# Performance work log

Measured on AMD Instinct MI355X. Metric: run time of the kernel, lower is better.

## Reference

```python
import jax, jax.numpy as jnp
import numpy as np

IN_F = 4096
OUT_F = 4096
SPLIT_F = 410   # ceil(4096 * 0.1)
NUM_PARTS = 10  # ceil(4096 / 410)


def setup_inputs() -> dict:
    key = jax.random.key(0)
    ks = jax.random.split(key, 7)
    s = 1.0 / np.sqrt(IN_F)
    sn = 1.0 / np.sqrt(NUM_PARTS)
    return {
        'x': jax.random.normal(ks[0], (2, 2048, IN_F), dtype=jnp.float32),
        'Wsel': jax.random.uniform(ks[1], (NUM_PARTS, IN_F), jnp.float32, -s, s),
        'bsel': jax.random.uniform(ks[2], (NUM_PARTS,), jnp.float32, -s, s),
        'Wexp': jax.random.uniform(ks[3], (IN_F, NUM_PARTS), jnp.float32, -sn, sn),
        'bexp': jax.random.uniform(ks[4], (IN_F,), jnp.float32, -sn, sn),
        'Wfc': jax.random.uniform(ks[5], (SPLIT_F, IN_F), jnp.float32, -s, s),
        'bfc': jax.random.uniform(ks[6], (SPLIT_F,), jnp.float32, -s, s),
        'out_features': OUT_F,
    }


def reference(x, Wsel, bsel, Wexp, bexp, Wfc, bfc, out_features):
    # selector: sx[..., n]
    sx = jnp.einsum('bsi,ni->bsn', x, Wsel) + bsel
    # expander(diag_embed(sx)): px[..., n, f] = sx[..., n] * Wexp[f, n] + bexp[f]
    # (diag matrix never materialized; mathematically identical)
    px = sx[..., :, None] * Wexp.T[None, None, :, :] + bexp  # [b, s, n, in]
    xx = x[..., None, :] + px                                # broadcast-add of x
    y = jnp.einsum('bsni,fi->bsnf', xx, Wfc) + bfc           # splitfc, [b, s, n, sf]
    y = y.reshape(y.shape[0], y.shape[1], -1)                # (n sf) flatten
    return y[..., :out_features]
```

## Files before the change

### kernel.cpp

```cpp
#include <hip/hip_runtime.h>
#include <hip/hip_bf16.h>
#include <stdint.h>

#define TKS    4096
#define KD     4096
#define NSF    410
#define NPARTS 10
#define NPAD   512
#define OUTF   4096

#define BM 64
#define BN 64
#define BK 128

typedef unsigned short u16;
typedef __attribute__((ext_vector_type(8))) short bf16x8;
typedef __attribute__((ext_vector_type(4))) float f32x4;

#define WS_XB  0
#define WS_BSW ((size_t)TKS * KD * 2)
#define WS_G   (WS_BSW + (size_t)NPAD * KD * 2)
#define WS_C   (WS_G + (size_t)NPAD * NPARTS * 4)
#define WS_SX  (WS_C + (size_t)NPAD * 4)
#define WS_WT  (WS_SX + (size_t)TKS * NPARTS * 4)

__device__ inline u16 f2bf(float f) {
    union { __hip_bfloat16 b; u16 u; } cv;
    cv.b = __float2bfloat16(f);
    return cv.u;
}

typedef __attribute__((address_space(3))) unsigned int as3_uint;
typedef __attribute__((address_space(1))) unsigned int as1_uint;
__device__ inline void gl_lds16(const void* g, void* l) {
    __builtin_amdgcn_global_load_lds((as1_uint*)(uintptr_t)g,
                                     (as3_uint*)(uintptr_t)l, 16, 0, 0);
}

__device__ inline int g_row(int g) { int s = g >> 6; return (s >> 2) * 32 + (s & 1) * 16 + (g & 15); }
__device__ inline int g_col(int g) { int s = g >> 6; return ((s >> 1) & 1) * 32 + ((g >> 4) & 3) * 8; }

__global__ __launch_bounds__(256) void retile_x(const float* __restrict__ x,
                                                u16* __restrict__ xb) {
    const int kt = blockIdx.x & 63, tb = blockIdx.x >> 6;
    const int tid = threadIdx.x;
    const float* tin = x + (size_t)(tb * 64) * KD + kt * 64;
    u16* tout = xb + ((size_t)(tb * 64 + kt) * 512) * 8;
#pragma unroll
    for (int j = 0; j < 2; ++j) {
        const int g = j * 256 + tid;
        const int r = g_row(g), cg = g_col(g);
        float4 v0 = *(const float4*)&tin[(size_t)r * KD + cg];
        float4 v1 = *(const float4*)&tin[(size_t)r * KD + cg + 4];
        u16 h[8] = { f2bf(v0.x), f2bf(v0.y), f2bf(v0.z), f2bf(v0.w),
                     f2bf(v1.x), f2bf(v1.y), f2bf(v1.z), f2bf(v1.w) };
        *(uint4*)&tout[(size_t)g * 8] = *(uint4*)h;
    }
}

__global__ __launch_bounds__(256) void retile_b(const float* __restrict__ Wfc,
                                                u16* __restrict__ bsw) {
    const int kt = blockIdx.x & 63, rb = blockIdx.x >> 6;
    const int tid = threadIdx.x;
    u16* tout = bsw + ((size_t)(rb * 64 + kt) * 512) * 8;
#pragma unroll
    for (int j = 0; j < 2; ++j) {
        const int g = j * 256 + tid;
        const int r = rb * 64 + g_row(g);
        uint4 pk = make_uint4(0u, 0u, 0u, 0u);
        if (r < NSF) {
            const float* src = Wfc + (size_t)r * KD + kt * 64 + g_col(g);
            float4 v0 = *(const float4*)src;
            float4 v1 = *(const float4*)(src + 4);
            u16 h[8] = { f2bf(v0.x), f2bf(v0.y), f2bf(v0.z), f2bf(v0.w),
                         f2bf(v1.x), f2bf(v1.y), f2bf(v1.z), f2bf(v1.w) };
            pk = *(uint4*)h;
        }
        *(uint4*)&tout[(size_t)g * 8] = pk;
    }
}

__global__ __launch_bounds__(256) void sel_kernel(const float* __restrict__ x,
                                                  const float* __restrict__ Wsel,
                                                  const float* __restrict__ bsel,
                                                  float* __restrict__ sx) {
    __shared__ float wsl[NPARTS][512];
    const int tid  = threadIdx.x;
    const int lane = tid & 63;
    const int w    = tid >> 6;
    const int t0   = blockIdx.x * 8 + w * 2;

    float acc0[NPARTS], acc1[NPARTS];
#pragma unroll
    for (int n = 0; n < NPARTS; ++n) { acc0[n] = 0.f; acc1[n] = 0.f; }

    const float* xr0 = x + (size_t)t0 * KD;
    const float* xr1 = xr0 + KD;

    for (int ch = 0; ch < 8; ++ch) {
        __syncthreads();
#pragma unroll
        for (int it = 0; it < 5; ++it) {
            int idx = it * 256 + tid;
            int n = idx >> 7, c4 = (idx & 127) * 4;
            *(float4*)&wsl[n][c4] = *(const float4*)&Wsel[n * KD + ch * 512 + c4];
        }
        __syncthreads();
#pragma unroll
        for (int j = 0; j < 2; ++j) {
            int kl = j * 256 + lane * 4;
            float4 x0 = *(const float4*)&xr0[ch * 512 + kl];
            float4 x1 = *(const float4*)&xr1[ch * 512 + kl];
#pragma unroll
            for (int n = 0; n < NPARTS; ++n) {
                float4 wv = *(float4*)&wsl[n][kl];
                acc0[n] += x0.x * wv.x + x0.y * wv.y + x0.z * wv.z + x0.w * wv.w;
                acc1[n] += x1.x * wv.x + x1.y * wv.y + x1.z * wv.z + x1.w * wv.w;
            }
        }
    }
#pragma unroll
    for (int off = 32; off >= 1; off >>= 1)
#pragma unroll
        for (int n = 0; n < NPARTS; ++n) {
            acc0[n] += __shfl_xor(acc0[n], off);
            acc1[n] += __shfl_xor(acc1[n], off);
        }
    if (lane == 0) {
#pragma unroll
        for (int n = 0; n < NPARTS; ++n) {
            float bs = bsel[n];
            sx[(size_t)t0 * NPARTS + n]       = acc0[n] + bs;
            sx[(size_t)(t0 + 1) * NPARTS + n] = acc1[n] + bs;
        }
    }
}

__global__ __launch_bounds__(256) void prep_a(const float* __restrict__ Wexp,
                                              const float* __restrict__ bexp,
                                              float* __restrict__ WT) {
    const int k = blockIdx.x * 256 + threadIdx.x;
#pragma unroll
    for (int n = 0; n < NPARTS; ++n) WT[(size_t)n * KD + k] = Wexp[(size_t)k * NPARTS + n];
    WT[(size_t)NPARTS * KD + k] = bexp[k];
}

__global__ __launch_bounds__(256) void prep_b(const float* __restrict__ Wfc,
                                              const float* __restrict__ bfc,
                                              const float* __restrict__ WT,
                                              float* __restrict__ G,
                                              float* __restrict__ c) {
    const int f = blockIdx.x;
    const int tid = threadIdx.x;
    float acc[NPARTS + 1];
#pragma unroll
    for (int n = 0; n <= NPARTS; ++n) acc[n] = 0.f;

#pragma unroll
    for (int i = 0; i < 4; ++i) {
        const int k = i * 1024 + tid * 4;
        float4 wv = *(const float4*)&Wfc[(size_t)f * KD + k];
#pragma unroll
        for (int n = 0; n <= NPARTS; ++n) {
            float4 t = *(const float4*)&WT[(size_t)n * KD + k];
            acc[n] += wv.x * t.x + wv.y * t.y + wv.z * t.z + wv.w * t.w;
        }
    }
#pragma unroll
    for (int off = 32; off >= 1; off >>= 1)
#pragma unroll
        for (int n = 0; n <= NPARTS; ++n) acc[n] += __shfl_xor(acc[n], off);

    __shared__ float red[4][NPARTS + 1];
    const int w = tid >> 6, lane = tid & 63;
    if (lane == 0) {
#pragma unroll
        for (int n = 0; n <= NPARTS; ++n) red[w][n] = acc[n];
    }
    __syncthreads();
    if (tid < NPARTS)
        G[(size_t)f * NPARTS + tid] = red[0][tid] + red[1][tid] + red[2][tid] + red[3][tid];
    if (tid == NPARTS)
        c[f] = red[0][NPARTS] + red[1][NPARTS] + red[2][NPARTS] + red[3][NPARTS] + bfc[f];
}

__global__ __launch_bounds__(256, 2) void main_kernel(const u16* __restrict__ xb,
                                                      const u16* __restrict__ bsw,
                                                      const float* __restrict__ G,
                                                      const float* __restrict__ cvec,
                                                      const float* __restrict__ sx,
                                                      float* __restrict__ out) {
    __shared__ __align__(16) u16 As[2][8192];
    __shared__ __align__(16) u16 Bs[2][8192];
    __shared__ float sxs[BM][NPARTS];
    __shared__ float Gs[BN][NPARTS];
    __shared__ float cs[BN];

    const int tid = threadIdx.x;
    const int fb  = blockIdx.x >> 6;
    const int tb  = blockIdx.x & 63;

    const int lane = tid & 63;
    const int w  = tid >> 6;
    const int wr = w >> 1, wc = w & 1;
    const int q  = lane >> 4, ml = lane & 15;

    f32x4 acc[2][2];
#pragma unroll
    for (int mi = 0; mi < 2; ++mi)
#pragma unroll
        for (int ni = 0; ni < 2; ++ni) acc[mi][ni] = (f32x4){0.f, 0.f, 0.f, 0.f};

    const u16* abase = xb  + (size_t)tb * 64 * 4096;
    const u16* bbase = bsw + (size_t)fb * 64 * 4096;

    for (int idx = tid; idx < BM * NPARTS; idx += 256)
        sxs[idx / NPARTS][idx % NPARTS] = sx[(size_t)(tb * BM + idx / NPARTS) * NPARTS + idx % NPARTS];
    for (int idx = tid; idx < BN * NPARTS; idx += 256)
        Gs[idx / NPARTS][idx % NPARTS] = G[(size_t)(fb * BN + idx / NPARTS) * NPARTS + idx % NPARTS];
    if (tid < BN) cs[tid] = cvec[fb * BN + tid];

#pragma unroll
    for (int k = 0; k < 4; ++k) {
        gl_lds16(abase + (k * 256 + tid) * 8, &As[0][(k * 256 + tid) * 8]);
        gl_lds16(bbase + (k * 256 + tid) * 8, &Bs[0][(k * 256 + tid) * 8]);
    }
    __syncthreads();

    int buf = 0;
#pragma unroll 2
    for (int it = 0; it < KD / BK; ++it) {
        if (it + 1 < KD / BK) {
            const size_t off = (size_t)(it + 1) * 8192;
#pragma unroll
            for (int k = 0; k < 4; ++k) {
                gl_lds16(abase + off + (k * 256 + tid) * 8, &As[buf ^ 1][(k * 256 + tid) * 8]);
                gl_lds16(bbase + off + (k * 256 + tid) * 8, &Bs[buf ^ 1][(k * 256 + tid) * 8]);
            }
        }
#pragma unroll
        for (int ks = 0; ks < 4; ++ks) {
            const int tb2 = (ks >> 1) * 512;
            const int kl  = ks & 1;
            bf16x8 av[2], bv[2];
#pragma unroll
            for (int mi = 0; mi < 2; ++mi)
                av[mi] = *(const bf16x8*)&As[buf][(tb2 + ((wr * 2 + kl) * 2 + mi) * 64 + lane) * 8];
#pragma unroll
            for (int ni = 0; ni < 2; ++ni)
                bv[ni] = *(const bf16x8*)&Bs[buf][(tb2 + ((wc * 2 + kl) * 2 + ni) * 64 + lane) * 8];
#pragma unroll
            for (int mi = 0; mi < 2; ++mi)
#pragma unroll
                for (int ni = 0; ni < 2; ++ni)
                    acc[mi][ni] = __builtin_amdgcn_mfma_f32_16x16x32_bf16(
                        av[mi], bv[ni], acc[mi][ni], 0, 0, 0);
        }
        __syncthreads();
        buf ^= 1;
    }

#pragma unroll
    for (int ni = 0; ni < 2; ++ni) {
        const int fl = wc * 32 + ni * 16 + ml;
        const int fg = fb * BN + fl;
        if (fg >= NSF) continue;
        const float cv = cs[fl];
        float gv[NPARTS];
#pragma unroll
        for (int n = 0; n < NPARTS; ++n) gv[n] = Gs[fl][n];
#pragma unroll
        for (int mi = 0; mi < 2; ++mi) {
#pragma unroll
            for (int r = 0; r < 4; ++r) {
                const int tl = wr * 32 + mi * 16 + q * 4 + r;
                const float av = acc[mi][ni][r] + cv;
                float* orow = out + (size_t)(tb * BM + tl) * OUTF;
#pragma unroll
                for (int n = 0; n < NPARTS; ++n) {
                    int j = n * NSF + fg;
                    if (j < OUTF) orow[j] = av + sxs[tl][n] * gv[n];
                }
            }
        }
    }
}

extern "C" void kernel_launch(void* const* d_in, const int* in_sizes, int n_in,
                              void* d_out, int out_size, void* d_ws, size_t ws_size,
                              hipStream_t stream) {
    const float* x    = (const float*)d_in[0];
    const float* Wsel = (const float*)d_in[1];
    const float* bsel = (const float*)d_in[2];
    const float* Wexp = (const float*)d_in[3];
    const float* bexp = (const float*)d_in[4];
    const float* Wfc  = (const float*)d_in[5];
    const float* bfc  = (const float*)d_in[6];
    float* out = (float*)d_out;

    char* ws = (char*)d_ws;
    u16*   xb   = (u16*)  (ws + WS_XB);
    u16*   bsw  = (u16*)  (ws + WS_BSW);
    float* G    = (float*)(ws + WS_G);
    float* c    = (float*)(ws + WS_C);
    float* sx   = (float*)(ws + WS_SX);
    float* WT   = (float*)(ws + WS_WT);

    prep_a<<<dim3(16), dim3(256), 0, stream>>>(Wexp, bexp, WT);
    retile_b<<<dim3(7 * 64), dim3(256), 0, stream>>>(Wfc, bsw);
    prep_b<<<dim3(NSF), dim3(256), 0, stream>>>(Wfc, bfc, WT, G, c);
    sel_kernel<<<dim3(TKS / 8), dim3(256), 0, stream>>>(x, Wsel, bsel, sx);
    retile_x<<<dim3(64 * 64), dim3(256), 0, stream>>>(x, xb);
    main_kernel<<<dim3(7 * 64), dim3(256), 0, stream>>>(xb, bsw, G, c, sx, out);
}
```

Baseline: 224.3 us.

## Fuse selector GEMV with x bf16 retiling and weight prep kernels

Merges the selector projection and the x-to-bf16 retile into one kernel so x is read from global memory once instead of twice. Also merges the Wfc retile with the G/c weight precomputation into a 28-block kernel that writes per-K-chunk partial sums, which main_kernel adds together when it loads G and c. This cuts six launches down to three and removes redundant reads of x and Wfc. In exchange, fuse_w runs on only 28 blocks, which may leave most CUs idle, and fuse_x uses shared-memory atomics.

```diff
diff --git a/kernel.cpp b/kernel.cpp
--- a/kernel.cpp
+++ b/kernel.cpp
@@ -19,10 +19,8 @@
 
 #define WS_XB  0
 #define WS_BSW ((size_t)TKS * KD * 2)
-#define WS_G   (WS_BSW + (size_t)NPAD * KD * 2)
-#define WS_C   (WS_G + (size_t)NPAD * NPARTS * 4)
-#define WS_SX  (WS_C + (size_t)NPAD * 4)
-#define WS_WT  (WS_SX + (size_t)TKS * NPARTS * 4)
+#define WS_GP  (WS_BSW + (size_t)NPAD * KD * 2)
+#define WS_SX  (WS_GP + (size_t)4 * NPAD * 12 * 4)
 
 __device__ inline u16 f2bf(float f) {
     union { __hip_bfloat16 b; u16 u; } cv;
@@ -37,157 +35,151 @@
                                      (as3_uint*)(uintptr_t)l, 16, 0, 0);
 }
 
-__device__ inline int g_row(int g) { int s = g >> 6; return (s >> 2) * 32 + (s & 1) * 16 + (g & 15); }
-__device__ inline int g_col(int g) { int s = g >> 6; return ((s >> 1) & 1) * 32 + ((g >> 4) & 3) * 8; }
-
-__global__ __launch_bounds__(256) void retile_x(const float* __restrict__ x,
-                                                u16* __restrict__ xb) {
-    const int kt = blockIdx.x & 63, tb = blockIdx.x >> 6;
+
+__global__ __launch_bounds__(256) void fuse_x(const float* __restrict__ x,
+                                              const float* __restrict__ Wsel,
+                                              const float* __restrict__ bsel,
+                                              u16* __restrict__ xb,
+                                              float* __restrict__ sx) {
+    __shared__ float wsl[NPARTS][1024];
+    __shared__ float sxp[8][NPARTS];
+
     const int tid = threadIdx.x;
-    const float* tin = x + (size_t)(tb * 64) * KD + kt * 64;
-    u16* tout = xb + ((size_t)(tb * 64 + kt) * 512) * 8;
-#pragma unroll
-    for (int j = 0; j < 2; ++j) {
-        const int g = j * 256 + tid;
-        const int r = g_row(g), cg = g_col(g);
-        float4 v0 = *(const float4*)&tin[(size_t)r * KD + cg];
-        float4 v1 = *(const float4*)&tin[(size_t)r * KD + cg + 4];
-        u16 h[8] = { f2bf(v0.x), f2bf(v0.y), f2bf(v0.z), f2bf(v0.w),
-                     f2bf(v1.x), f2bf(v1.y), f2bf(v1.z), f2bf(v1.w) };
-        *(uint4*)&tout[(size_t)g * 8] = *(uint4*)h;
-    }
-}
-
-__global__ __launch_bounds__(256) void retile_b(const float* __restrict__ Wfc,
-                                                u16* __restrict__ bsw) {
-    const int kt = blockIdx.x & 63, rb = blockIdx.x >> 6;
-    const int tid = threadIdx.x;
-    u16* tout = bsw + ((size_t)(rb * 64 + kt) * 512) * 8;
-#pragma unroll
-    for (int j = 0; j < 2; ++j) {
-        const int g = j * 256 + tid;
-        const int r = rb * 64 + g_row(g);
-        uint4 pk = make_uint4(0u, 0u, 0u, 0u);
-        if (r < NSF) {
-            const float* src = Wfc + (size_t)r * KD + kt * 64 + g_col(g);
-            float4 v0 = *(const float4*)src;
-            float4 v1 = *(const float4*)(src + 4);
+    const int b   = blockIdx.x;
+    const int c   = tid & 7;
+    const int r   = (tid >> 3) & 7;
+    const int kq  = tid >> 6;
+
+    const int tb = b >> 3, b7 = b & 7;
+    const int hi = b7 >> 2, lo = (b7 >> 1) & 1, ml = (b7 & 1) * 8 + r;
+    const int slot = hi * 4 + (c >> 2) * 2 + lo;
+    const int g    = slot * 64 + (c & 3) * 16 + ml;
+
+    if (tid < 8 * NPARTS) sxp[tid / NPARTS][tid % NPARTS] = 0.f;
+
+    float acc[NPARTS];
+#pragma unroll
+    for (int n = 0; n < NPARTS; ++n) acc[n] = 0.f;
+
+    const float* xrow = x + (size_t)(b * 8 + r) * KD;
+
+    for (int st = 0; st < 4; ++st) {
+        __syncthreads();
+#pragma unroll
+        for (int it = 0; it < 10; ++it) {
+            int idx = it * 256 + tid;
+            int n = idx >> 8, c4 = (idx & 255) * 4;
+            *(float4*)&wsl[n][c4] = *(const float4*)&Wsel[n * KD + st * 1024 + c4];
+        }
+        __syncthreads();
+#pragma unroll
+        for (int i2 = 0; i2 < 4; ++i2) {
+            const int ktl = (st * 4 + i2) * 4 + kq;
+            const int kg  = ktl * 64 + c * 8;
+            float4 v0 = *(const float4*)&xrow[kg];
+            float4 v1 = *(const float4*)&xrow[kg + 4];
             u16 h[8] = { f2bf(v0.x), f2bf(v0.y), f2bf(v0.z), f2bf(v0.w),
                          f2bf(v1.x), f2bf(v1.y), f2bf(v1.z), f2bf(v1.w) };
-            pk = *(uint4*)h;
-        }
-        *(uint4*)&tout[(size_t)g * 8] = pk;
-    }
-}
-
-__global__ __launch_bounds__(256) void sel_kernel(const float* __restrict__ x,
-                                                  const float* __restrict__ Wsel,
-                                                  const float* __restrict__ bsel,
-                                                  float* __restrict__ sx) {
-    __shared__ float wsl[NPARTS][512];
-    const int tid  = threadIdx.x;
-    const int lane = tid & 63;
-    const int w    = tid >> 6;
-    const int t0   = blockIdx.x * 8 + w * 2;
-
-    float acc0[NPARTS], acc1[NPARTS];
-#pragma unroll
-    for (int n = 0; n < NPARTS; ++n) { acc0[n] = 0.f; acc1[n] = 0.f; }
-
-    const float* xr0 = x + (size_t)t0 * KD;
-    const float* xr1 = xr0 + KD;
-
-    for (int ch = 0; ch < 8; ++ch) {
-        __syncthreads();
-#pragma unroll
-        for (int it = 0; it < 5; ++it) {
-            int idx = it * 256 + tid;
-            int n = idx >> 7, c4 = (idx & 127) * 4;
-            *(float4*)&wsl[n][c4] = *(const float4*)&Wsel[n * KD + ch * 512 + c4];
-        }
-        __syncthreads();
-#pragma unroll
-        for (int j = 0; j < 2; ++j) {
-            int kl = j * 256 + lane * 4;
-            float4 x0 = *(const float4*)&xr0[ch * 512 + kl];
-            float4 x1 = *(const float4*)&xr1[ch * 512 + kl];
+            *(uint4*)&xb[((size_t)(tb * 64 + ktl) * 512 + g) * 8] = *(uint4*)h;
+            const int cloc = (i2 * 4 + kq) * 64 + c * 8;
 #pragma unroll
             for (int n = 0; n < NPARTS; ++n) {
-                float4 wv = *(float4*)&wsl[n][kl];
-                acc0[n] += x0.x * wv.x + x0.y * wv.y + x0.z * wv.z + x0.w * wv.w;
-                acc1[n] += x1.x * wv.x + x1.y * wv.y + x1.z * wv.z + x1.w * wv.w;
-            }
-        }
-    }
-#pragma unroll
-    for (int off = 32; off >= 1; off >>= 1)
-#pragma unroll
-        for (int n = 0; n < NPARTS; ++n) {
-            acc0[n] += __shfl_xor(acc0[n], off);
-            acc1[n] += __shfl_xor(acc1[n], off);
-        }
-    if (lane == 0) {
-#pragma unroll
-        for (int n = 0; n < NPARTS; ++n) {
-            float bs = bsel[n];
-            sx[(size_t)t0 * NPARTS + n]       = acc0[n] + bs;
-            sx[(size_t)(t0 + 1) * NPARTS + n] = acc1[n] + bs;
-        }
-    }
-}
-
-__global__ __launch_bounds__(256) void prep_a(const float* __restrict__ Wexp,
+                float4 w0 = *(float4*)&wsl[n][cloc];
+                float4 w1 = *(float4*)&wsl[n][cloc + 4];
+                acc[n] += v0.x * w0.x + v0.y * w0.y + v0.z * w0.z + v0.w * w0.w
+                        + v1.x * w1.x + v1.y * w1.y + v1.z * w1.z + v1.w * w1.w;
+            }
+        }
+    }
+    __syncthreads();
+#pragma unroll
+    for (int n = 0; n < NPARTS; ++n) atomicAdd(&sxp[r][n], acc[n]);
+    __syncthreads();
+    if (tid < 8 * NPARTS)
+        sx[(size_t)(b * 8 + tid / NPARTS) * NPARTS + tid % NPARTS] =
+            sxp[tid / NPARTS][tid % NPARTS] + bsel[tid % NPARTS];
+}
+
+__global__ __launch_bounds__(256) void fuse_w(const float* __restrict__ Wfc,
+                                              const float* __restrict__ Wexp,
                                               const float* __restrict__ bexp,
-                                              float* __restrict__ WT) {
-    const int k = blockIdx.x * 256 + threadIdx.x;
-#pragma unroll
-    for (int n = 0; n < NPARTS; ++n) WT[(size_t)n * KD + k] = Wexp[(size_t)k * NPARTS + n];
-    WT[(size_t)NPARTS * KD + k] = bexp[k];
-}
-
-__global__ __launch_bounds__(256) void prep_b(const float* __restrict__ Wfc,
-                                              const float* __restrict__ bfc,
-                                              const float* __restrict__ WT,
-                                              float* __restrict__ G,
-                                              float* __restrict__ c) {
-    const int f = blockIdx.x;
+                                              u16* __restrict__ bsw,
+                                              float* __restrict__ Gpart) {
+    __shared__ float cmb[1024 * 12];
+
     const int tid = threadIdx.x;
-    float acc[NPARTS + 1];
-#pragma unroll
-    for (int n = 0; n <= NPARTS; ++n) acc[n] = 0.f;
-
-#pragma unroll
-    for (int i = 0; i < 4; ++i) {
-        const int k = i * 1024 + tid * 4;
-        float4 wv = *(const float4*)&Wfc[(size_t)f * KD + k];
-#pragma unroll
-        for (int n = 0; n <= NPARTS; ++n) {
-            float4 t = *(const float4*)&WT[(size_t)n * KD + k];
-            acc[n] += wv.x * t.x + wv.y * t.y + wv.z * t.z + wv.w * t.w;
-        }
-    }
-#pragma unroll
-    for (int off = 32; off >= 1; off >>= 1)
-#pragma unroll
-        for (int n = 0; n <= NPARTS; ++n) acc[n] += __shfl_xor(acc[n], off);
-
-    __shared__ float red[4][NPARTS + 1];
-    const int w = tid >> 6, lane = tid & 63;
-    if (lane == 0) {
-#pragma unroll
-        for (int n = 0; n <= NPARTS; ++n) red[w][n] = acc[n];
-    }
+    const int rb = blockIdx.x >> 2, kc = blockIdx.x & 3;
+
+    for (int idx = tid; idx < 1024 * NPARTS; idx += 256)
+        cmb[(idx / NPARTS) * 12 + (idx % NPARTS)] = Wexp[(size_t)kc * 1024 * NPARTS + idx];
+    for (int idx = tid; idx < 1024; idx += 256)
+        cmb[idx * 12 + 10] = bexp[kc * 1024 + idx];
     __syncthreads();
-    if (tid < NPARTS)
-        G[(size_t)f * NPARTS + tid] = red[0][tid] + red[1][tid] + red[2][tid] + red[3][tid];
-    if (tid == NPARTS)
-        c[f] = red[0][NPARTS] + red[1][NPARTS] + red[2][NPARTS] + red[3][NPARTS] + bfc[f];
+
+    const int c = tid & 7, rr = tid >> 3;
+    float acc[2][12];
+#pragma unroll
+    for (int hh = 0; hh < 2; ++hh)
+#pragma unroll
+        for (int n = 0; n < 12; ++n) acc[hh][n] = 0.f;
+
+    for (int j = 0; j < 16; ++j) {
+        const int ktg = kc * 16 + j;
+#pragma unroll
+        for (int hh = 0; hh < 2; ++hh) {
+            const int lr  = rr + hh * 32;
+            const int row = rb * 64 + lr;
+            float4 v0 = make_float4(0.f, 0.f, 0.f, 0.f);
+            float4 v1 = make_float4(0.f, 0.f, 0.f, 0.f);
+            if (row < NSF) {
+                const float* src = Wfc + (size_t)row * KD + ktg * 64 + c * 8;
+                v0 = *(const float4*)src;
+                v1 = *(const float4*)(src + 4);
+            }
+            u16 h[8] = { f2bf(v0.x), f2bf(v0.y), f2bf(v0.z), f2bf(v0.w),
+                         f2bf(v1.x), f2bf(v1.y), f2bf(v1.z), f2bf(v1.w) };
+            const int g = ((lr >> 5) * 4 + (c >> 2) * 2 + ((lr >> 4) & 1)) * 64
+                        + (c & 3) * 16 + (lr & 15);
+            *(uint4*)&bsw[((size_t)(rb * 64 + ktg) * 512 + g) * 8] = *(uint4*)h;
+
+            const float w[8] = { v0.x, v0.y, v0.z, v0.w, v1.x, v1.y, v1.z, v1.w };
+            const int cl = j * 64 + c * 8;
+#pragma unroll
+            for (int jj = 0; jj < 8; ++jj) {
+                const float* cb = &cmb[(cl + jj) * 12];
+                float4 a0 = *(float4*)cb;
+                float4 a1 = *(float4*)(cb + 4);
+                float4 a2 = *(float4*)(cb + 8);
+                acc[hh][0] += w[jj] * a0.x;  acc[hh][1] += w[jj] * a0.y;
+                acc[hh][2] += w[jj] * a0.z;  acc[hh][3] += w[jj] * a0.w;
+                acc[hh][4] += w[jj] * a1.x;  acc[hh][5] += w[jj] * a1.y;
+                acc[hh][6] += w[jj] * a1.z;  acc[hh][7] += w[jj] * a1.w;
+                acc[hh][8] += w[jj] * a2.x;  acc[hh][9] += w[jj] * a2.y;
+                acc[hh][10] += w[jj] * a2.z;
+            }
+        }
+    }
+#pragma unroll
+    for (int m = 1; m <= 4; m <<= 1)
+#pragma unroll
+        for (int hh = 0; hh < 2; ++hh)
+#pragma unroll
+            for (int n = 0; n < 11; ++n) acc[hh][n] += __shfl_xor(acc[hh][n], m);
+    if (c == 0) {
+#pragma unroll
+        for (int hh = 0; hh < 2; ++hh) {
+            const int f = rb * 64 + rr + hh * 32;
+#pragma unroll
+            for (int n = 0; n < 11; ++n)
+                Gpart[((size_t)kc * NPAD + f) * 12 + n] = acc[hh][n];
+        }
+    }
 }
 
 __global__ __launch_bounds__(256, 2) void main_kernel(const u16* __restrict__ xb,
                                                       const u16* __restrict__ bsw,
-                                                      const float* __restrict__ G,
-                                                      const float* __restrict__ cvec,
+                                                      const float* __restrict__ Gpart,
+                                                      const float* __restrict__ bfc,
                                                       const float* __restrict__ sx,
                                                       float* __restrict__ out) {
     __shared__ __align__(16) u16 As[2][8192];
@@ -216,9 +208,22 @@
 
     for (int idx = tid; idx < BM * NPARTS; idx += 256)
         sxs[idx / NPARTS][idx % NPARTS] = sx[(size_t)(tb * BM + idx / NPARTS) * NPARTS + idx % NPARTS];
-    for (int idx = tid; idx < BN * NPARTS; idx += 256)
-        Gs[idx / NPARTS][idx % NPARTS] = G[(size_t)(fb * BN + idx / NPARTS) * NPARTS + idx % NPARTS];
-    if (tid < BN) cs[tid] = cvec[fb * BN + tid];
+    for (int idx = tid; idx < BN * NPARTS; idx += 256) {
+        const int fl = idx / NPARTS, n = idx % NPARTS;
+        const int fg = fb * BN + fl;
+        Gs[fl][n] = Gpart[((size_t)0 * NPAD + fg) * 12 + n]
+                  + Gpart[((size_t)1 * NPAD + fg) * 12 + n]
+                  + Gpart[((size_t)2 * NPAD + fg) * 12 + n]
+                  + Gpart[((size_t)3 * NPAD + fg) * 12 + n];
+    }
+    if (tid < BN) {
+        const int fg = fb * BN + tid;
+        float s = Gpart[((size_t)0 * NPAD + fg) * 12 + 10]
+                + Gpart[((size_t)1 * NPAD + fg) * 12 + 10]
+                + Gpart[((size_t)2 * NPAD + fg) * 12 + 10]
+                + Gpart[((size_t)3 * NPAD + fg) * 12 + 10];
+        cs[tid] = s + (fg < NSF ? bfc[fg] : 0.f);
+    }
 
 #pragma unroll
     for (int k = 0; k < 4; ++k) {
@@ -299,17 +304,12 @@
     float* out = (float*)d_out;
 
     char* ws = (char*)d_ws;
-    u16*   xb   = (u16*)  (ws + WS_XB);
-    u16*   bsw  = (u16*)  (ws + WS_BSW);
-    float* G    = (float*)(ws + WS_G);
-    float* c    = (float*)(ws + WS_C);
-    float* sx   = (float*)(ws + WS_SX);
-    float* WT   = (float*)(ws + WS_WT);
-
-    prep_a<<<dim3(16), dim3(256), 0, stream>>>(Wexp, bexp, WT);
-    retile_b<<<dim3(7 * 64), dim3(256), 0, stream>>>(Wfc, bsw);
-    prep_b<<<dim3(NSF), dim3(256), 0, stream>>>(Wfc, bfc, WT, G, c);
-    sel_kernel<<<dim3(TKS / 8), dim3(256), 0, stream>>>(x, Wsel, bsel, sx);
-    retile_x<<<dim3(64 * 64), dim3(256), 0, stream>>>(x, xb);
-    main_kernel<<<dim3(7 * 64), dim3(256), 0, stream>>>(xb, bsw, G, c, sx, out);
-}
+    u16*   xb    = (u16*)  (ws + WS_XB);
+    u16*   bsw   = (u16*)  (ws + WS_BSW);
+    float* Gpart = (float*)(ws + WS_GP);
+    float* sx    = (float*)(ws + WS_SX);
+
+    fuse_w<<<dim3(28), dim3(256), 0, stream>>>(Wfc, Wexp, bexp, bsw, Gpart);
+    fuse_x<<<dim3(512), dim3(256), 0, stream>>>(x, Wsel, bsel, xb, sx);
+    main_kernel<<<dim3(7 * 64), dim3(256), 0, stream>>>(xb, bsw, Gpart, bfc, sx, out);
+}
```

After: 242.1 us. 1.08x slower.

## Fuse x bf16 conversion into GEMM main loop, dropping retile_x pass

Applied to the files above, without the earlier changes.

Removes the separate retile_x kernel that converted and retiled x to bf16 in workspace. The GEMM now loads fp32 x directly into registers, converts to bf16 and stores to LDS after the MFMA stage, replacing the async global-to-LDS loads with register prefetch. This avoids a full write and re-read of the bf16 copy of x. In exchange, each column block re-reads fp32 x at twice the bytes, and register pressure in the main loop rises.

```diff
diff --git a/kernel.cpp b/kernel.cpp
--- a/kernel.cpp
+++ b/kernel.cpp
@@ -17,9 +17,8 @@
 typedef __attribute__((ext_vector_type(8))) short bf16x8;
 typedef __attribute__((ext_vector_type(4))) float f32x4;
 
-#define WS_XB  0
-#define WS_BSW ((size_t)TKS * KD * 2)
-#define WS_G   (WS_BSW + (size_t)NPAD * KD * 2)
+#define WS_BSW 0
+#define WS_G   ((size_t)NPAD * KD * 2)
 #define WS_C   (WS_G + (size_t)NPAD * NPARTS * 4)
 #define WS_SX  (WS_C + (size_t)NPAD * 4)
 #define WS_WT  (WS_SX + (size_t)TKS * NPARTS * 4)
@@ -30,32 +29,16 @@
     return cv.u;
 }
 
-typedef __attribute__((address_space(3))) unsigned int as3_uint;
-typedef __attribute__((address_space(1))) unsigned int as1_uint;
-__device__ inline void gl_lds16(const void* g, void* l) {
-    __builtin_amdgcn_global_load_lds((as1_uint*)(uintptr_t)g,
-                                     (as3_uint*)(uintptr_t)l, 16, 0, 0);
-}
-
 __device__ inline int g_row(int g) { int s = g >> 6; return (s >> 2) * 32 + (s & 1) * 16 + (g & 15); }
 __device__ inline int g_col(int g) { int s = g >> 6; return ((s >> 1) & 1) * 32 + ((g >> 4) & 3) * 8; }
 
-__global__ __launch_bounds__(256) void retile_x(const float* __restrict__ x,
-                                                u16* __restrict__ xb) {
-    const int kt = blockIdx.x & 63, tb = blockIdx.x >> 6;
-    const int tid = threadIdx.x;
-    const float* tin = x + (size_t)(tb * 64) * KD + kt * 64;
-    u16* tout = xb + ((size_t)(tb * 64 + kt) * 512) * 8;
-#pragma unroll
-    for (int j = 0; j < 2; ++j) {
-        const int g = j * 256 + tid;
-        const int r = g_row(g), cg = g_col(g);
-        float4 v0 = *(const float4*)&tin[(size_t)r * KD + cg];
-        float4 v1 = *(const float4*)&tin[(size_t)r * KD + cg + 4];
-        u16 h[8] = { f2bf(v0.x), f2bf(v0.y), f2bf(v0.z), f2bf(v0.w),
-                     f2bf(v1.x), f2bf(v1.y), f2bf(v1.z), f2bf(v1.w) };
-        *(uint4*)&tout[(size_t)g * 8] = *(uint4*)h;
-    }
+__global__ __launch_bounds__(256) void prep_a(const float* __restrict__ Wexp,
+                                              const float* __restrict__ bexp,
+                                              float* __restrict__ WT) {
+    const int k = blockIdx.x * 256 + threadIdx.x;
+#pragma unroll
+    for (int n = 0; n < NPARTS; ++n) WT[(size_t)n * KD + k] = Wexp[(size_t)k * NPARTS + n];
+    WT[(size_t)NPARTS * KD + k] = bexp[k];
 }
 
 __global__ __launch_bounds__(256) void retile_b(const float* __restrict__ Wfc,
@@ -80,6 +63,45 @@
     }
 }
 
+__global__ __launch_bounds__(256) void prep_b(const float* __restrict__ Wfc,
+                                              const float* __restrict__ bfc,
+                                              const float* __restrict__ WT,
+                                              float* __restrict__ G,
+                                              float* __restrict__ c) {
+    const int f = blockIdx.x;
+    const int tid = threadIdx.x;
+    float acc[NPARTS + 1];
+#pragma unroll
+    for (int n = 0; n <= NPARTS; ++n) acc[n] = 0.f;
+
+#pragma unroll
+    for (int i = 0; i < 4; ++i) {
+        const int k = i * 1024 + tid * 4;
+        float4 wv = *(const float4*)&Wfc[(size_t)f * KD + k];
+#pragma unroll
+        for (int n = 0; n <= NPARTS; ++n) {
+            float4 t = *(const float4*)&WT[(size_t)n * KD + k];
+            acc[n] += wv.x * t.x + wv.y * t.y + wv.z * t.z + wv.w * t.w;
+        }
+    }
+#pragma unroll
+    for (int off = 32; off >= 1; off >>= 1)
+#pragma unroll
+        for (int n = 0; n <= NPARTS; ++n) acc[n] += __shfl_xor(acc[n], off);
+
+    __shared__ float red[4][NPARTS + 1];
+    const int w = tid >> 6, lane = tid & 63;
+    if (lane == 0) {
+#pragma unroll
+        for (int n = 0; n <= NPARTS; ++n) red[w][n] = acc[n];
+    }
+    __syncthreads();
+    if (tid < NPARTS)
+        G[(size_t)f * NPARTS + tid] = red[0][tid] + red[1][tid] + red[2][tid] + red[3][tid];
+    if (tid == NPARTS)
+        c[f] = red[0][NPARTS] + red[1][NPARTS] + red[2][NPARTS] + red[3][NPARTS] + bfc[f];
+}
+
 __global__ __launch_bounds__(256) void sel_kernel(const float* __restrict__ x,
                                                   const float* __restrict__ Wsel,
                                                   const float* __restrict__ bsel,
@@ -136,56 +158,8 @@
     }
 }
 
-__global__ __launch_bounds__(256) void prep_a(const float* __restrict__ Wexp,
-                                              const float* __restrict__ bexp,
-                                              float* __restrict__ WT) {
-    const int k = blockIdx.x * 256 + threadIdx.x;
-#pragma unroll
-    for (int n = 0; n < NPARTS; ++n) WT[(size_t)n * KD + k] = Wexp[(size_t)k * NPARTS + n];
-    WT[(size_t)NPARTS * KD + k] = bexp[k];
-}
-
-__global__ __launch_bounds__(256) void prep_b(const float* __restrict__ Wfc,
-                                              const float* __restrict__ bfc,
-                                              const float* __restrict__ WT,
-                                              float* __restrict__ G,
-                                              float* __restrict__ c) {
-    const int f = blockIdx.x;
-    const int tid = threadIdx.x;
-    float acc[NPARTS + 1];
-#pragma unroll
-    for (int n = 0; n <= NPARTS; ++n) acc[n] = 0.f;
-
-#pragma unroll
-    for (int i = 0; i < 4; ++i) {
-        const int k = i * 1024 + tid * 4;
-        float4 wv = *(const float4*)&Wfc[(size_t)f * KD + k];
-#pragma unroll
-        for (int n = 0; n <= NPARTS; ++n) {
-            float4 t = *(const float4*)&WT[(size_t)n * KD + k];
-            acc[n] += wv.x * t.x + wv.y * t.y + wv.z * t.z + wv.w * t.w;
-        }
-    }
-#pragma unroll
-    for (int off = 32; off >= 1; off >>= 1)
-#pragma unroll
-        for (int n = 0; n <= NPARTS; ++n) acc[n] += __shfl_xor(acc[n], off);
-
-    __shared__ float red[4][NPARTS + 1];
-    const int w = tid >> 6, lane = tid & 63;
-    if (lane == 0) {
-#pragma unroll
-        for (int n = 0; n <= NPARTS; ++n) red[w][n] = acc[n];
-    }
-    __syncthreads();
-    if (tid < NPARTS)
-        G[(size_t)f * NPARTS + tid] = red[0][tid] + red[1][tid] + red[2][tid] + red[3][tid];
-    if (tid == NPARTS)
-        c[f] = red[0][NPARTS] + red[1][NPARTS] + red[2][NPARTS] + red[3][NPARTS] + bfc[f];
-}
-
-__global__ __launch_bounds__(256, 2) void main_kernel(const u16* __restrict__ xb,
-                                                      const u16* __restrict__ bsw,
+__global__ __launch_bounds__(256, 2) void main_kernel(const float* __restrict__ x,
+                                                      const u16*   __restrict__ bsw,
                                                       const float* __restrict__ G,
                                                       const float* __restrict__ cvec,
                                                       const float* __restrict__ sx,
@@ -211,8 +185,18 @@
 #pragma unroll
         for (int ni = 0; ni < 2; ++ni) acc[mi][ni] = (f32x4){0.f, 0.f, 0.f, 0.f};
 
-    const u16* abase = xb  + (size_t)tb * 64 * 4096;
-    const u16* bbase = bsw + (size_t)fb * 64 * 4096;
+    const float* aptr[4];
+    const u16*   bptr[4];
+    int go[4];
+#pragma unroll
+    for (int j = 0; j < 4; ++j) {
+        const int gg = j * 256 + tid;
+        const int tile = gg >> 9;
+        const int gl   = gg & 511;
+        aptr[j] = x + (size_t)(tb * 64 + g_row(gl)) * KD + tile * 64 + g_col(gl);
+        bptr[j] = bsw + ((size_t)(fb * 64 + tile) * 512 + gl) * 8;
+        go[j] = gg * 8;
+    }
 
     for (int idx = tid; idx < BM * NPARTS; idx += 256)
         sxs[idx / NPARTS][idx % NPARTS] = sx[(size_t)(tb * BM + idx / NPARTS) * NPARTS + idx % NPARTS];
@@ -220,22 +204,34 @@
         Gs[idx / NPARTS][idx % NPARTS] = G[(size_t)(fb * BN + idx / NPARTS) * NPARTS + idx % NPARTS];
     if (tid < BN) cs[tid] = cvec[fb * BN + tid];
 
-#pragma unroll
-    for (int k = 0; k < 4; ++k) {
-        gl_lds16(abase + (k * 256 + tid) * 8, &As[0][(k * 256 + tid) * 8]);
-        gl_lds16(bbase + (k * 256 + tid) * 8, &Bs[0][(k * 256 + tid) * 8]);
+    float4 a0[4], a1[4];
+    uint4  bq[4];
+#pragma unroll
+    for (int j = 0; j < 4; ++j) {
+        a0[j] = *(const float4*)(aptr[j]);
+        a1[j] = *(const float4*)(aptr[j] + 4);
+        bq[j] = *(const uint4*)(bptr[j]);
+    }
+#pragma unroll
+    for (int j = 0; j < 4; ++j) {
+        u16 h[8] = { f2bf(a0[j].x), f2bf(a0[j].y), f2bf(a0[j].z), f2bf(a0[j].w),
+                     f2bf(a1[j].x), f2bf(a1[j].y), f2bf(a1[j].z), f2bf(a1[j].w) };
+        *(uint4*)&As[0][go[j]] = *(uint4*)h;
+        *(uint4*)&Bs[0][go[j]] = bq[j];
     }
     __syncthreads();
 
     int buf = 0;
 #pragma unroll 2
     for (int it = 0; it < KD / BK; ++it) {
-        if (it + 1 < KD / BK) {
-            const size_t off = (size_t)(it + 1) * 8192;
-#pragma unroll
-            for (int k = 0; k < 4; ++k) {
-                gl_lds16(abase + off + (k * 256 + tid) * 8, &As[buf ^ 1][(k * 256 + tid) * 8]);
-                gl_lds16(bbase + off + (k * 256 + tid) * 8, &Bs[buf ^ 1][(k * 256 + tid) * 8]);
+        const bool pre = (it + 1) < KD / BK;
+        if (pre) {
+            const int ko = (it + 1) * BK;
+#pragma unroll
+            for (int j = 0; j < 4; ++j) {
+                a0[j] = *(const float4*)(aptr[j] + ko);
+                a1[j] = *(const float4*)(aptr[j] + ko + 4);
+                bq[j] = *(const uint4*)(bptr[j] + (size_t)(it + 1) * 8192);
             }
         }
 #pragma unroll
@@ -255,6 +251,15 @@
                 for (int ni = 0; ni < 2; ++ni)
                     acc[mi][ni] = __builtin_amdgcn_mfma_f32_16x16x32_bf16(
                         av[mi], bv[ni], acc[mi][ni], 0, 0, 0);
+        }
+        if (pre) {
+#pragma unroll
+            for (int j = 0; j < 4; ++j) {
+                u16 h[8] = { f2bf(a0[j].x), f2bf(a0[j].y), f2bf(a0[j].z), f2bf(a0[j].w),
+                             f2bf(a1[j].x), f2bf(a1[j].y), f2bf(a1[j].z), f2bf(a1[j].w) };
+                *(uint4*)&As[buf ^ 1][go[j]] = *(uint4*)h;
+                *(uint4*)&Bs[buf ^ 1][go[j]] = bq[j];
+            }
         }
         __syncthreads();
         buf ^= 1;
@@ -299,7 +304,6 @@
     float* out = (float*)d_out;
 
     char* ws = (char*)d_ws;
-    u16*   xb   = (u16*)  (ws + WS_XB);
     u16*   bsw  = (u16*)  (ws + WS_BSW);
     float* G    = (float*)(ws + WS_G);
     float* c    = (float*)(ws + WS_C);
@@ -310,6 +314,5 @@
     retile_b<<<dim3(7 * 64), dim3(256), 0, stream>>>(Wfc, bsw);
     prep_b<<<dim3(NSF), dim3(256), 0, stream>>>(Wfc, bfc, WT, G, c);
     sel_kernel<<<dim3(TKS / 8), dim3(256), 0, stream>>>(x, Wsel, bsel, sx);
-    retile_x<<<dim3(64 * 64), dim3(256), 0, stream>>>(x, xb);
-    main_kernel<<<dim3(7 * 64), dim3(256), 0, stream>>>(xb, bsw, G, c, sx, out);
-}
+    main_kernel<<<dim3(7 * 64), dim3(256), 0, stream>>>(x, bsw, G, c, sx, out);
+}
```

Result: slower. 289.3 us (+29.0%).

## Fuse selector and Wfc·Wexp projections into main GEMM via extra MFMAs

Applied to the files above, without the earlier changes.

Removes the separate sel_kernel, prep_a and prep_b launches. The selector outputs (x·Wsel) and the folded G = Wfc·Wexp and c vectors are now computed inside main_kernel with extra bf16 MFMAs on the tiles already in LDS. The tile shrinks to BM=32, BK=64 with 4 blocks per CU, doubling the grid to improve occupancy. In exchange, sx and G are now computed in bf16 instead of fp32, which loses precision, and the G/c work is recomputed redundantly by every token block.

```diff
diff --git a/kernel.cpp b/kernel.cpp
--- a/kernel.cpp
+++ b/kernel.cpp
@@ -6,12 +6,11 @@
 #define KD     4096
 #define NSF    410
 #define NPARTS 10
-#define NPAD   512
 #define OUTF   4096
 
-#define BM 64
+#define BM 32
 #define BN 64
-#define BK 128
+#define BK 64
 
 typedef unsigned short u16;
 typedef __attribute__((ext_vector_type(8))) short bf16x8;
@@ -19,10 +18,8 @@
 
 #define WS_XB  0
 #define WS_BSW ((size_t)TKS * KD * 2)
-#define WS_G   (WS_BSW + (size_t)NPAD * KD * 2)
-#define WS_C   (WS_G + (size_t)NPAD * NPARTS * 4)
-#define WS_SX  (WS_C + (size_t)NPAD * 4)
-#define WS_WT  (WS_SX + (size_t)TKS * NPARTS * 4)
+#define WS_WSL (WS_BSW + (size_t)512 * KD * 2)
+#define WS_WEX (WS_WSL + (size_t)16 * KD * 2)
 
 __device__ inline u16 f2bf(float f) {
     union { __hip_bfloat16 b; u16 u; } cv;
@@ -40,21 +37,28 @@
 __device__ inline int g_row(int g) { int s = g >> 6; return (s >> 2) * 32 + (s & 1) * 16 + (g & 15); }
 __device__ inline int g_col(int g) { int s = g >> 6; return ((s >> 1) & 1) * 32 + ((g >> 4) & 3) * 8; }
 
-__global__ __launch_bounds__(256) void retile_x(const float* __restrict__ x,
-                                                u16* __restrict__ xb) {
-    const int kt = blockIdx.x & 63, tb = blockIdx.x >> 6;
+__global__ __launch_bounds__(256) void prep_w(const float* __restrict__ Wsel,
+                                              const float* __restrict__ Wexp,
+                                              const float* __restrict__ bexp,
+                                              u16* __restrict__ wselb,
+                                              u16* __restrict__ wexpb) {
+    const int kt = blockIdx.x;
     const int tid = threadIdx.x;
-    const float* tin = x + (size_t)(tb * 64) * KD + kt * 64;
-    u16* tout = xb + ((size_t)(tb * 64 + kt) * 512) * 8;
-#pragma unroll
-    for (int j = 0; j < 2; ++j) {
-        const int g = j * 256 + tid;
-        const int r = g_row(g), cg = g_col(g);
-        float4 v0 = *(const float4*)&tin[(size_t)r * KD + cg];
-        float4 v1 = *(const float4*)&tin[(size_t)r * KD + cg + 4];
-        u16 h[8] = { f2bf(v0.x), f2bf(v0.y), f2bf(v0.z), f2bf(v0.w),
-                     f2bf(v1.x), f2bf(v1.y), f2bf(v1.z), f2bf(v1.w) };
-        *(uint4*)&tout[(size_t)g * 8] = *(uint4*)h;
+    const int g  = tid & 127;
+    const int ml = g & 15;
+    const int col = kt * 64 + (g >> 6) * 32 + ((g >> 4) & 3) * 8;
+    u16 h[8];
+    if (tid < 128) {
+#pragma unroll
+        for (int j = 0; j < 8; ++j)
+            h[j] = (ml < NPARTS) ? f2bf(Wsel[(size_t)ml * KD + col + j]) : (u16)0;
+        *(uint4*)&wselb[((size_t)kt * 128 + g) * 8] = *(uint4*)h;
+    } else {
+#pragma unroll
+        for (int j = 0; j < 8; ++j)
+            h[j] = (ml < NPARTS) ? f2bf(Wexp[(size_t)(col + j) * NPARTS + ml])
+                 : (ml == NPARTS ? f2bf(bexp[col + j]) : (u16)0);
+        *(uint4*)&wexpb[((size_t)kt * 128 + g) * 8] = *(uint4*)h;
     }
 }
 
@@ -80,185 +84,114 @@
     }
 }
 
-__global__ __launch_bounds__(256) void sel_kernel(const float* __restrict__ x,
-                                                  const float* __restrict__ Wsel,
-                                                  const float* __restrict__ bsel,
-                                                  float* __restrict__ sx) {
-    __shared__ float wsl[NPARTS][512];
-    const int tid  = threadIdx.x;
-    const int lane = tid & 63;
-    const int w    = tid >> 6;
-    const int t0   = blockIdx.x * 8 + w * 2;
-
-    float acc0[NPARTS], acc1[NPARTS];
-#pragma unroll
-    for (int n = 0; n < NPARTS; ++n) { acc0[n] = 0.f; acc1[n] = 0.f; }
-
-    const float* xr0 = x + (size_t)t0 * KD;
-    const float* xr1 = xr0 + KD;
-
-    for (int ch = 0; ch < 8; ++ch) {
-        __syncthreads();
-#pragma unroll
-        for (int it = 0; it < 5; ++it) {
-            int idx = it * 256 + tid;
-            int n = idx >> 7, c4 = (idx & 127) * 4;
-            *(float4*)&wsl[n][c4] = *(const float4*)&Wsel[n * KD + ch * 512 + c4];
-        }
-        __syncthreads();
-#pragma unroll
-        for (int j = 0; j < 2; ++j) {
-            int kl = j * 256 + lane * 4;
-            float4 x0 = *(const float4*)&xr0[ch * 512 + kl];
-            float4 x1 = *(const float4*)&xr1[ch * 512 + kl];
-#pragma unroll
-            for (int n = 0; n < NPARTS; ++n) {
-                float4 wv = *(float4*)&wsl[n][kl];
-                acc0[n] += x0.x * wv.x + x0.y * wv.y + x0.z * wv.z + x0.w * wv.w;
-                acc1[n] += x1.x * wv.x + x1.y * wv.y + x1.z * wv.z + x1.w * wv.w;
-            }
-        }
-    }
-#pragma unroll
-    for (int off = 32; off >= 1; off >>= 1)
-#pragma unroll
-        for (int n = 0; n < NPARTS; ++n) {
-            acc0[n] += __shfl_xor(acc0[n], off);
-            acc1[n] += __shfl_xor(acc1[n], off);
-        }
-    if (lane == 0) {
-#pragma unroll
-        for (int n = 0; n < NPARTS; ++n) {
-            float bs = bsel[n];
-            sx[(size_t)t0 * NPARTS + n]       = acc0[n] + bs;
-            sx[(size_t)(t0 + 1) * NPARTS + n] = acc1[n] + bs;
-        }
-    }
-}
-
-__global__ __launch_bounds__(256) void prep_a(const float* __restrict__ Wexp,
-                                              const float* __restrict__ bexp,
-                                              float* __restrict__ WT) {
-    const int k = blockIdx.x * 256 + threadIdx.x;
-#pragma unroll
-    for (int n = 0; n < NPARTS; ++n) WT[(size_t)n * KD + k] = Wexp[(size_t)k * NPARTS + n];
-    WT[(size_t)NPARTS * KD + k] = bexp[k];
-}
-
-__global__ __launch_bounds__(256) void prep_b(const float* __restrict__ Wfc,
-                                              const float* __restrict__ bfc,
-                                              const float* __restrict__ WT,
-                                              float* __restrict__ G,
-                                              float* __restrict__ c) {
-    const int f = blockIdx.x;
-    const int tid = threadIdx.x;
-    float acc[NPARTS + 1];
-#pragma unroll
-    for (int n = 0; n <= NPARTS; ++n) acc[n] = 0.f;
-
-#pragma unroll
-    for (int i = 0; i < 4; ++i) {
-        const int k = i * 1024 + tid * 4;
-        float4 wv = *(const float4*)&Wfc[(size_t)f * KD + k];
-#pragma unroll
-        for (int n = 0; n <= NPARTS; ++n) {
-            float4 t = *(const float4*)&WT[(size_t)n * KD + k];
-            acc[n] += wv.x * t.x + wv.y * t.y + wv.z * t.z + wv.w * t.w;
-        }
-    }
-#pragma unroll
-    for (int off = 32; off >= 1; off >>= 1)
-#pragma unroll
-        for (int n = 0; n <= NPARTS; ++n) acc[n] += __shfl_xor(acc[n], off);
-
-    __shared__ float red[4][NPARTS + 1];
-    const int w = tid >> 6, lane = tid & 63;
-    if (lane == 0) {
-#pragma unroll
-        for (int n = 0; n <= NPARTS; ++n) red[w][n] = acc[n];
-    }
-    __syncthreads();
-    if (tid < NPARTS)
-        G[(size_t)f * NPARTS + tid] = red[0][tid] + red[1][tid] + red[2][tid] + red[3][tid];
-    if (tid == NPARTS)
-        c[f] = red[0][NPARTS] + red[1][NPARTS] + red[2][NPARTS] + red[3][NPARTS] + bfc[f];
-}
-
-__global__ __launch_bounds__(256, 2) void main_kernel(const u16* __restrict__ xb,
+__global__ __launch_bounds__(256) void retile_x(const float* __restrict__ x,
+                                                u16* __restrict__ xb) {
+    const int kt = blockIdx.x & 63, tb = blockIdx.x >> 6;
+    const int g = threadIdx.x;
+    const int slot = g >> 6;
+    const int row = (slot & 1) * 16 + (g & 15);
+    const int col = (slot >> 1) * 32 + ((g >> 4) & 3) * 8;
+    const float* src = x + (size_t)(tb * 32 + row) * KD + kt * 64 + col;
+    float4 v0 = *(const float4*)src;
+    float4 v1 = *(const float4*)(src + 4);
+    u16 h[8] = { f2bf(v0.x), f2bf(v0.y), f2bf(v0.z), f2bf(v0.w),
+                 f2bf(v1.x), f2bf(v1.y), f2bf(v1.z), f2bf(v1.w) };
+    *(uint4*)&xb[((size_t)(tb * 64 + kt) * 256 + g) * 8] = *(uint4*)h;
+}
+
+__global__ __launch_bounds__(256, 4) void main_kernel(const u16* __restrict__ xb,
                                                       const u16* __restrict__ bsw,
-                                                      const float* __restrict__ G,
-                                                      const float* __restrict__ cvec,
-                                                      const float* __restrict__ sx,
+                                                      const u16* __restrict__ wselb,
+                                                      const u16* __restrict__ wexpb,
+                                                      const float* __restrict__ bsel,
+                                                      const float* __restrict__ bfc,
                                                       float* __restrict__ out) {
-    __shared__ __align__(16) u16 As[2][8192];
-    __shared__ __align__(16) u16 Bs[2][8192];
+    __shared__ __align__(16) u16 As[2][2048];
+    __shared__ __align__(16) u16 Bs[2][4096];
+    __shared__ __align__(16) u16 Wl[2][1024];
+    __shared__ __align__(16) u16 We[2][1024];
     __shared__ float sxs[BM][NPARTS];
     __shared__ float Gs[BN][NPARTS];
     __shared__ float cs[BN];
 
     const int tid = threadIdx.x;
-    const int fb  = blockIdx.x >> 6;
-    const int tb  = blockIdx.x & 63;
+    const int fb  = blockIdx.x >> 7;
+    const int tb  = blockIdx.x & 127;
 
     const int lane = tid & 63;
     const int w  = tid >> 6;
-    const int wr = w >> 1, wc = w & 1;
+    const int mt = w & 1, wc = w >> 1;
     const int q  = lane >> 4, ml = lane & 15;
 
-    f32x4 acc[2][2];
-#pragma unroll
-    for (int mi = 0; mi < 2; ++mi)
-#pragma unroll
-        for (int ni = 0; ni < 2; ++ni) acc[mi][ni] = (f32x4){0.f, 0.f, 0.f, 0.f};
-
-    const u16* abase = xb  + (size_t)tb * 64 * 4096;
-    const u16* bbase = bsw + (size_t)fb * 64 * 4096;
-
-    for (int idx = tid; idx < BM * NPARTS; idx += 256)
-        sxs[idx / NPARTS][idx % NPARTS] = sx[(size_t)(tb * BM + idx / NPARTS) * NPARTS + idx % NPARTS];
-    for (int idx = tid; idx < BN * NPARTS; idx += 256)
-        Gs[idx / NPARTS][idx % NPARTS] = G[(size_t)(fb * BN + idx / NPARTS) * NPARTS + idx % NPARTS];
-    if (tid < BN) cs[tid] = cvec[fb * BN + tid];
-
-#pragma unroll
-    for (int k = 0; k < 4; ++k) {
-        gl_lds16(abase + (k * 256 + tid) * 8, &As[0][(k * 256 + tid) * 8]);
-        gl_lds16(bbase + (k * 256 + tid) * 8, &Bs[0][(k * 256 + tid) * 8]);
-    }
+    f32x4 acc[2]   = { (f32x4){0.f,0.f,0.f,0.f}, (f32x4){0.f,0.f,0.f,0.f} };
+    f32x4 accsx    = (f32x4){0.f,0.f,0.f,0.f};
+    f32x4 accG[2]  = { (f32x4){0.f,0.f,0.f,0.f}, (f32x4){0.f,0.f,0.f,0.f} };
+
+    const u16* ab = xb  + (size_t)tb * 131072;
+    const u16* bb = bsw + (size_t)fb * 262144;
+
+    gl_lds16(ab + tid * 8, &As[0][tid * 8]);
+    gl_lds16(bb + tid * 8, &Bs[0][tid * 8]);
+    gl_lds16(bb + (256 + tid) * 8, &Bs[0][(256 + tid) * 8]);
+    if (tid < 128) gl_lds16(wselb + tid * 8, &Wl[0][tid * 8]);
+    else           gl_lds16(wexpb + (tid - 128) * 8, &We[0][(tid - 128) * 8]);
     __syncthreads();
 
     int buf = 0;
 #pragma unroll 2
     for (int it = 0; it < KD / BK; ++it) {
         if (it + 1 < KD / BK) {
-            const size_t off = (size_t)(it + 1) * 8192;
-#pragma unroll
-            for (int k = 0; k < 4; ++k) {
-                gl_lds16(abase + off + (k * 256 + tid) * 8, &As[buf ^ 1][(k * 256 + tid) * 8]);
-                gl_lds16(bbase + off + (k * 256 + tid) * 8, &Bs[buf ^ 1][(k * 256 + tid) * 8]);
-            }
-        }
-#pragma unroll
-        for (int ks = 0; ks < 4; ++ks) {
-            const int tb2 = (ks >> 1) * 512;
-            const int kl  = ks & 1;
-            bf16x8 av[2], bv[2];
-#pragma unroll
-            for (int mi = 0; mi < 2; ++mi)
-                av[mi] = *(const bf16x8*)&As[buf][(tb2 + ((wr * 2 + kl) * 2 + mi) * 64 + lane) * 8];
-#pragma unroll
-            for (int ni = 0; ni < 2; ++ni)
-                bv[ni] = *(const bf16x8*)&Bs[buf][(tb2 + ((wc * 2 + kl) * 2 + ni) * 64 + lane) * 8];
-#pragma unroll
-            for (int mi = 0; mi < 2; ++mi)
-#pragma unroll
-                for (int ni = 0; ni < 2; ++ni)
-                    acc[mi][ni] = __builtin_amdgcn_mfma_f32_16x16x32_bf16(
-                        av[mi], bv[ni], acc[mi][ni], 0, 0, 0);
+            const size_t ao = (size_t)(it + 1) * 2048;
+            const size_t bo = (size_t)(it + 1) * 4096;
+            const size_t wo = (size_t)(it + 1) * 1024;
+            gl_lds16(ab + ao + tid * 8, &As[buf ^ 1][tid * 8]);
+            gl_lds16(bb + bo + tid * 8, &Bs[buf ^ 1][tid * 8]);
+            gl_lds16(bb + bo + (256 + tid) * 8, &Bs[buf ^ 1][(256 + tid) * 8]);
+            if (tid < 128) gl_lds16(wselb + wo + tid * 8, &Wl[buf ^ 1][tid * 8]);
+            else           gl_lds16(wexpb + wo + (tid - 128) * 8, &We[buf ^ 1][(tid - 128) * 8]);
+        }
+#pragma unroll
+        for (int ks = 0; ks < 2; ++ks) {
+            bf16x8 av  = *(const bf16x8*)&As[buf][((ks * 2 + mt) * 64 + lane) * 8];
+            bf16x8 bv0 = *(const bf16x8*)&Bs[buf][((wc * 4 + ks * 2 + 0) * 64 + lane) * 8];
+            bf16x8 bv1 = *(const bf16x8*)&Bs[buf][((wc * 4 + ks * 2 + 1) * 64 + lane) * 8];
+            acc[0] = __builtin_amdgcn_mfma_f32_16x16x32_bf16(av, bv0, acc[0], 0, 0, 0);
+            acc[1] = __builtin_amdgcn_mfma_f32_16x16x32_bf16(av, bv1, acc[1], 0, 0, 0);
+            if (wc == 0) {
+                bf16x8 wf = *(const bf16x8*)&Wl[buf][(ks * 64 + lane) * 8];
+                accsx = __builtin_amdgcn_mfma_f32_16x16x32_bf16(av, wf, accsx, 0, 0, 0);
+            }
+            if (mt == 0) {
+                bf16x8 ef = *(const bf16x8*)&We[buf][(ks * 64 + lane) * 8];
+                accG[0] = __builtin_amdgcn_mfma_f32_16x16x32_bf16(bv0, ef, accG[0], 0, 0, 0);
+                accG[1] = __builtin_amdgcn_mfma_f32_16x16x32_bf16(bv1, ef, accG[1], 0, 0, 0);
+            }
         }
         __syncthreads();
         buf ^= 1;
     }
+
+    if (wc == 0 && ml < NPARTS) {
+        const float bs = bsel[ml];
+#pragma unroll
+        for (int r = 0; r < 4; ++r)
+            sxs[mt * 16 + q * 4 + r][ml] = accsx[r] + bs;
+    }
+    if (mt == 0) {
+#pragma unroll
+        for (int ni = 0; ni < 2; ++ni) {
+#pragma unroll
+            for (int r = 0; r < 4; ++r) {
+                const int f = wc * 32 + ni * 16 + q * 4 + r;
+                if (ml < NPARTS) Gs[f][ml] = accG[ni][r];
+                else if (ml == NPARTS) {
+                    const int fg = fb * BN + f;
+                    cs[f] = accG[ni][r] + (fg < NSF ? bfc[fg] : 0.f);
+                }
+            }
+        }
+    }
+    __syncthreads();
 
 #pragma unroll
     for (int ni = 0; ni < 2; ++ni) {
@@ -270,17 +203,14 @@
 #pragma unroll
         for (int n = 0; n < NPARTS; ++n) gv[n] = Gs[fl][n];
 #pragma unroll
-        for (int mi = 0; mi < 2; ++mi) {
-#pragma unroll
-            for (int r = 0; r < 4; ++r) {
-                const int tl = wr * 32 + mi * 16 + q * 4 + r;
-                const float av = acc[mi][ni][r] + cv;
-                float* orow = out + (size_t)(tb * BM + tl) * OUTF;
-#pragma unroll
-                for (int n = 0; n < NPARTS; ++n) {
-                    int j = n * NSF + fg;
-                    if (j < OUTF) orow[j] = av + sxs[tl][n] * gv[n];
-                }
+        for (int r = 0; r < 4; ++r) {
+            const int tl = mt * 16 + q * 4 + r;
+            const float av = acc[ni][r] + cv;
+            float* orow = out + (size_t)(tb * BM + tl) * OUTF;
+#pragma unroll
+            for (int n = 0; n < NPARTS; ++n) {
+                int j = n * NSF + fg;
+                if (j < OUTF) orow[j] = av + sxs[tl][n] * gv[n];
             }
         }
     }
@@ -299,17 +229,14 @@
     float* out = (float*)d_out;
 
     char* ws = (char*)d_ws;
-    u16*   xb   = (u16*)  (ws + WS_XB);
-    u16*   bsw  = (u16*)  (ws + WS_BSW);
-    float* G    = (float*)(ws + WS_G);
-    float* c    = (float*)(ws + WS_C);
-    float* sx   = (float*)(ws + WS_SX);
-    float* WT   = (float*)(ws + WS_WT);
-
-    prep_a<<<dim3(16), dim3(256), 0, stream>>>(Wexp, bexp, WT);
+    u16* xb    = (u16*)(ws + WS_XB);
+    u16* bsw   = (u16*)(ws + WS_BSW);
+    u16* wselb = (u16*)(ws + WS_WSL);
+    u16* wexpb = (u16*)(ws + WS_WEX);
+
+    prep_w<<<dim3(64), dim3(256), 0, stream>>>(Wsel, Wexp, bexp, wselb, wexpb);
     retile_b<<<dim3(7 * 64), dim3(256), 0, stream>>>(Wfc, bsw);
-    prep_b<<<dim3(NSF), dim3(256), 0, stream>>>(Wfc, bfc, WT, G, c);
-    sel_kernel<<<dim3(TKS / 8), dim3(256), 0, stream>>>(x, Wsel, bsel, sx);
-    retile_x<<<dim3(64 * 64), dim3(256), 0, stream>>>(x, xb);
-    main_kernel<<<dim3(7 * 64), dim3(256), 0, stream>>>(xb, bsw, G, c, sx, out);
-}
+    retile_x<<<dim3(128 * 64), dim3(256), 0, stream>>>(x, xb);
+    main_kernel<<<dim3(7 * 128), dim3(256), 0, stream>>>(xb, bsw, wselb, wexpb,
+                                                         bsel, bfc, out);
+}
```

Result: faster. 202.1 us (-9.9%).
